# Kernel tuning notes

Measured on AMD Instinct MI355X. Metric: run time of the kernel, lower is better.

## Reference

```python
import jax, jax.numpy as jnp
import numpy as np

NUM_HEADS = 8
T = 8  # hardcoded temporal dim in the original forward
MD = 3  # max_displacement -> 7x7 window
EPS = 1e-12  # F.normalize eps


def l2_normalize(x, axis):
    n = jnp.sqrt(jnp.sum(x * x, axis=axis, keepdims=True))
    return x / jnp.maximum(n, EPS)


def correlation_7x7(q, k):
    # q, k: [B, C, H, W]; FlowNet-style correlation, kernel_size=1, max_disp=3.
    # out[b, u, v, h, w] = sum_c q[b,c,h,w] * k[b,c,h+u-3,w+v-3] (zero padded)
    B, C, H, W = q.shape
    kp = jnp.pad(k, ((0, 0), (0, 0), (MD, MD), (MD, MD)))
    outs = []
    for dy in range(2 * MD + 1):
        for dx in range(2 * MD + 1):
            ks = kp[:, :, dy:dy + H, dx:dx + W]
            outs.append(jnp.sum(q * ks, axis=1))  # [B, H, W]
    corr = jnp.stack(outs, axis=1)  # [B, 49, H, W]
    return corr.reshape(B, 2 * MD + 1, 2 * MD + 1, H, W)


def setup_inputs() -> dict:
    key = jax.random.key(0)
    ks = jax.random.split(key, 6)
    B, N, C = 8, 8192, 256
    hd = C // NUM_HEADS
    std = 0.02
    return {
        "x": jax.random.normal(ks[0], (B, N, C), dtype=jnp.float32),
        "w_qk": jax.random.normal(ks[1], (2 * C, C), dtype=jnp.float32) * std,
        "w_corr": jax.random.normal(ks[2], (hd, 49), dtype=jnp.float32) * std,
        "b_corr": jnp.zeros((hd,), dtype=jnp.float32),
        "w_proj": jax.random.normal(ks[3], (C, C), dtype=jnp.float32) * std,
        "b_proj": jnp.zeros((C,), dtype=jnp.float32),
    }


def reference(x, w_qk, w_corr, b_corr, w_proj, b_proj):
    B, N, C = x.shape
    nh = NUM_HEADS
    hd = C // nh
    H = int(np.sqrt(N // T))
    W = H

    # qk projection (no bias): [B, N, 2C] -> q, k each [B, nh, N, hd]
    qk = jnp.einsum('bnc,dc->bnd', x, w_qk)
    qk = qk.reshape(B, N, 2, nh, hd).transpose(2, 0, 3, 1, 4)
    q, k = qk[0], qk[1]

    # 'b n (t h w) d -> (b n) t d h w'
    q = q.reshape(B * nh, T, H, W, hd).transpose(0, 1, 4, 2, 3)
    k = k.reshape(B * nh, T, H, W, hd).transpose(0, 1, 4, 2, 3)

    # temporal postfix: k[t+1], last frame repeated
    k_post = jnp.concatenate([k[:, 1:], k[:, -1:]], axis=1)

    qp = q.reshape(B * nh * T, hd, H, W)
    kp = k_post.reshape(B * nh * T, hd, H, W)
    qp = l2_normalize(qp, axis=1)
    kp = l2_normalize(kp, axis=1)

    corr = correlation_7x7(qp, kp)  # [(B nh T), 7, 7, H, W]
    # 'b u v h w -> b (h w) (u v)'
    corr = corr.transpose(0, 3, 4, 1, 2).reshape(B * nh * T, H * W, 49)

    v = jnp.einsum('bpk,dk->bpd', corr, w_corr) + b_corr  # [(B nh T), HW, hd]

    # '(b n t) (h w) d -> b n (t h w) d' then 'b h n d -> b n (h d)'
    out = v.reshape(B, nh, T * H * W, hd).transpose(0, 2, 1, 3).reshape(B, N, C)
    out = jnp.einsum('bnc,dc->bnd', out, w_proj) + b_proj
    return out
```

## Files before the change

kernel.cpp:

```cpp
#include <hip/hip_runtime.h>

typedef _Float16 half8 __attribute__((ext_vector_type(8)));
typedef _Float16 half2v __attribute__((ext_vector_type(2)));
typedef float float4v __attribute__((ext_vector_type(4)));

__device__ __forceinline__ float dot2acc(unsigned a, unsigned b, float c) {
#if __has_builtin(__builtin_amdgcn_fdot2)
  return __builtin_amdgcn_fdot2(__builtin_bit_cast(half2v, a), __builtin_bit_cast(half2v, b), c, false);
#else
  half2v ha = __builtin_bit_cast(half2v, a);
  half2v hb = __builtin_bit_cast(half2v, b);
  c += (float)ha[0] * (float)hb[0];
  c += (float)ha[1] * (float)hb[1];
  return c;
#endif
}
__device__ __forceinline__ unsigned hscale(unsigned a, float s) {
  half2v ha = __builtin_bit_cast(half2v, a);
  half2v r;
  r[0] = (_Float16)((float)ha[0] * s);
  r[1] = (_Float16)((float)ha[1] * s);
  return __builtin_bit_cast(unsigned, r);
}
__device__ __forceinline__ unsigned pack2(float a, float b) {
  half2v h;
  h[0] = (_Float16)a;
  h[1] = (_Float16)b;
  return __builtin_bit_cast(unsigned, h);
}
__device__ __forceinline__ void gload_lds16(const void* g, void* l) {
  __builtin_amdgcn_global_load_lds((const __attribute__((address_space(1))) unsigned*)g,
                                   (__attribute__((address_space(3))) unsigned*)l, 16, 0, 0);
}

__global__ void cvt_all(const float4* __restrict__ x, const float4* __restrict__ wqk,
                        const float4* __restrict__ wpj,
                        ushort4* __restrict__ x16, ushort4* __restrict__ wqk16,
                        ushort4* __restrict__ wpj16) {
  int b = blockIdx.x;
  const float4* s;
  ushort4* d;
  int i;
  if (b < 16384) { s = x; d = x16; i = b * 256 + threadIdx.x; }
  else if (b < 16512) { s = wqk; d = wqk16; i = (b - 16384) * 256 + threadIdx.x; }
  else { s = wpj; d = wpj16; i = (b - 16512) * 256 + threadIdx.x; }
  float4 v = s[i];
  _Float16 a = (_Float16)v.x, bb = (_Float16)v.y, c = (_Float16)v.z, e = (_Float16)v.w;
  ushort4 o;
  o.x = __builtin_bit_cast(unsigned short, a);
  o.y = __builtin_bit_cast(unsigned short, bb);
  o.z = __builtin_bit_cast(unsigned short, c);
  o.w = __builtin_bit_cast(unsigned short, e);
  d[i] = o;
}

__global__ __launch_bounds__(256, 2)
void gemm_qk(const _Float16* __restrict__ A, const _Float16* __restrict__ Bw,
             _Float16* __restrict__ qo, _Float16* __restrict__ ko) {
  __shared__ _Float16 Ash[8192];
  __shared__ _Float16 Bsh[8192];
  const int tid = threadIdx.x;
  const int lane = tid & 63, w = tid >> 6;
  const int wm = w >> 1, wn = w & 1;
  const int ml = lane & 15, qd = lane >> 4;
  const int m0 = blockIdx.y * 128, n0 = blockIdx.x * 128;

  float4v acc[4][4];
  float4v z = {0.f, 0.f, 0.f, 0.f};
#pragma unroll
  for (int i = 0; i < 4; ++i)
#pragma unroll
    for (int j = 0; j < 4; ++j) acc[i][j] = z;

  const _Float16* Ap = A + (size_t)m0 * 256;
  const _Float16* Bp = Bw + (size_t)n0 * 256;
  const int gr = w * 64 + lane;
  const int row0 = gr >> 2, kb = gr & 3;

  {
    gload_lds16(Ap + row0 * 256 + kb * 8, Ash + (size_t)(w * 64) * 8);
    gload_lds16(Ap + (row0 + 64) * 256 + kb * 8, Ash + (size_t)(256 + w * 64) * 8);
    gload_lds16(Bp + row0 * 256 + kb * 8, Bsh + (size_t)(w * 64) * 8);
    gload_lds16(Bp + (row0 + 64) * 256 + kb * 8, Bsh + (size_t)(256 + w * 64) * 8);
  }
  __syncthreads();

#pragma unroll
  for (int kt = 0; kt < 8; ++kt) {
    const int cur = kt & 1;
    if (kt < 7) {
      const int k0 = (kt + 1) * 32;
      const int nb = (cur ^ 1) * 4096;
      gload_lds16(Ap + row0 * 256 + k0 + kb * 8, Ash + nb + (size_t)(w * 64) * 8);
      gload_lds16(Ap + (row0 + 64) * 256 + k0 + kb * 8, Ash + nb + (size_t)(256 + w * 64) * 8);
      gload_lds16(Bp + row0 * 256 + k0 + kb * 8, Bsh + nb + (size_t)(w * 64) * 8);
      gload_lds16(Bp + (row0 + 64) * 256 + k0 + kb * 8, Bsh + nb + (size_t)(256 + w * 64) * 8);
    }
    const _Float16* Ac = Ash + cur * 4096;
    const _Float16* Bc = Bsh + cur * 4096;
    half8 af[4], bf[4];
#pragma unroll
    for (int im = 0; im < 4; ++im) {
      af[im] = *(const half8*)(Ac + (wm * 64 + im * 16 + ml) * 32 + qd * 8);
      bf[im] = *(const half8*)(Bc + (wn * 64 + im * 16 + ml) * 32 + qd * 8);
    }
#pragma unroll
    for (int im = 0; im < 4; ++im)
#pragma unroll
      for (int in = 0; in < 4; ++in)
        acc[im][in] = __builtin_amdgcn_mfma_f32_16x16x32_f16(bf[in], af[im], acc[im][in], 0, 0, 0);
    __syncthreads();
  }

#pragma unroll
  for (int im = 0; im < 4; ++im) {
    int rowr = m0 + wm * 64 + im * 16 + ml;
    int b = rowr >> 13, n = rowr & 8191;
    int t = n >> 10, yx = n & 1023;
#pragma unroll
    for (int in = 0; in < 4; ++in) {
      int col = n0 + wn * 64 + in * 16 + qd * 4;
      int s = col >> 8, h = (col >> 5) & 7, j = col & 31;
      _Float16* dst = s ? ko : qo;
      int p = b * 64 + h * 8 + t;
      uint2 pk;
      pk.x = pack2(acc[im][in][0], acc[im][in][1]);
      pk.y = pack2(acc[im][in][2], acc[im][in][3]);
      *(uint2*)(dst + ((size_t)p * 1024 + yx) * 32 + j) = pk;
    }
  }
}

__global__ __launch_bounds__(256, 4)
void corr_kernel(const _Float16* __restrict__ q16, const _Float16* __restrict__ k16,
                 const float* __restrict__ wcorr, const float* __restrict__ bcorr,
                 _Float16* __restrict__ outp) {
  __shared__ uint4 smem[2304];
  __shared__ uint4 wcs[256];

  const int tid = threadIdx.x;
  const int bx = blockIdx.x;
  const int p = bx >> 2, tile = bx & 3;
  const int y0 = (tile >> 1) * 16, x0 = (tile & 1) * 16;
  const int b = p >> 6, h = (p >> 3) & 7, t = p & 7;
  const int pk = (t < 7) ? p + 1 : p;
  const int ty = tid >> 4, tx = tid & 15;

  _Float16* wch = (_Float16*)wcs;
  for (int idx = tid; idx < 2048; idx += 256) {
    int d = idx >> 6, kk = idx & 63;
    float v = (kk < 49) ? wcorr[d * 49 + kk] : (kk == 49 ? bcorr[d] : 0.f);
    wch[idx] = (_Float16)v;
  }

  const _Float16* kbase = k16 + (size_t)pk * 32768;
#pragma unroll
  for (int i = 0; i < 8; ++i) {
    int g = tid + i * 256;
    if (g < 1936) {
      int vec = g >> 2, part = g & 3;
      int ky = vec / 22, kx = vec - ky * 22;
      int gy = y0 + ky - 3, gx = x0 + kx - 3;
      uint4 val = make_uint4(0u, 0u, 0u, 0u);
      if (gy >= 0 && gy < 32 && gx >= 0 && gx < 32)
        val = *(const uint4*)(kbase + ((size_t)gy * 32 + gx) * 32 + part * 8);
      int slot = (vec << 2) | (part ^ (vec & 3) ^ ((vec >> 2) & 3));
      smem[slot] = val;
    }
  }
  __syncthreads();

  for (int v = tid; v < 484; v += 256) {
    int base = v << 2;
    int sw = (v & 3) ^ ((v >> 2) & 3);
    uint4 gg[4];
#pragma unroll
    for (int pq = 0; pq < 4; ++pq) gg[pq] = smem[base | (pq ^ sw)];
    float ss = 0.f;
#pragma unroll
    for (int pq = 0; pq < 4; ++pq) {
      const unsigned* u = (const unsigned*)&gg[pq];
#pragma unroll
      for (int e = 0; e < 4; ++e) ss = dot2acc(u[e], u[e], ss);
    }
    float sc = 1.f / fmaxf(sqrtf(ss), 1e-12f);
#pragma unroll
    for (int pq = 0; pq < 4; ++pq) {
      unsigned* u = (unsigned*)&gg[pq];
#pragma unroll
      for (int e = 0; e < 4; ++e) u[e] = hscale(u[e], sc);
      smem[base | (pq ^ sw)] = gg[pq];
    }
  }
  __syncthreads();

  const _Float16* qptr = q16 + (size_t)p * 32768 + ((size_t)(y0 + ty) * 32 + (x0 + tx)) * 32;
  uint4 qv[4];
#pragma unroll
  for (int i = 0; i < 4; ++i) qv[i] = *(const uint4*)(qptr + i * 8);
  unsigned* qu = (unsigned*)qv;
  float qss = 0.f;
#pragma unroll
  for (int e = 0; e < 16; ++e) qss = dot2acc(qu[e], qu[e], qss);
  float qsc = 1.f / fmaxf(sqrtf(qss), 1e-12f);
#pragma unroll
  for (int e = 0; e < 16; ++e) qu[e] = hscale(qu[e], qsc);

  float corr[49];
#pragma unroll
  for (int dy = 0; dy < 7; ++dy) {
#pragma unroll
    for (int dx = 0; dx < 7; ++dx) {
      int vec = (ty + dy) * 22 + (tx + dx);
      int base = vec << 2;
      int sw = (vec & 3) ^ ((vec >> 2) & 3);
      float c = 0.f;
#pragma unroll
      for (int pq = 0; pq < 4; ++pq) {
        uint4 kk = smem[base | (pq ^ sw)];
        const unsigned* ku = (const unsigned*)&kk;
#pragma unroll
        for (int e = 0; e < 4; ++e) c = dot2acc(qu[pq * 4 + e], ku[e], c);
      }
      corr[dy * 7 + dx] = c;
    }
  }
  __syncthreads();

#pragma unroll
  for (int i = 0; i < 8; ++i) {
    uint4 val;
    unsigned* vu = (unsigned*)&val;
#pragma unroll
    for (int e = 0; e < 4; ++e) {
      int idx = i * 8 + e * 2;
      half2v hh;
      hh[0] = (_Float16)(idx < 49 ? corr[idx] : (idx == 49 ? 1.f : 0.f));
      hh[1] = (_Float16)(idx + 1 < 49 ? corr[idx + 1] : (idx + 1 == 49 ? 1.f : 0.f));
      vu[e] = __builtin_bit_cast(unsigned, hh);
    }
    smem[tid * 9 + i] = val;
  }
  __syncthreads();

  _Float16* corrm = (_Float16*)smem;
  const int lane = tid & 63, w = tid >> 6;
  const int ml = lane & 15, qd = lane >> 4;
  float4v vacc[4][2];
  float4v z = {0.f, 0.f, 0.f, 0.f};
#pragma unroll
  for (int im = 0; im < 4; ++im) { vacc[im][0] = z; vacc[im][1] = z; }
#pragma unroll
  for (int ks = 0; ks < 2; ++ks) {
    half8 bfrag[2];
#pragma unroll
    for (int nt = 0; nt < 2; ++nt)
      bfrag[nt] = *(const half8*)(wch + (nt * 16 + ml) * 64 + ks * 32 + qd * 8);
#pragma unroll
    for (int im = 0; im < 4; ++im) {
      half8 afrag = *(const half8*)(corrm + (w * 64 + im * 16 + ml) * 72 + ks * 32 + qd * 8);
#pragma unroll
      for (int nt = 0; nt < 2; ++nt)
        vacc[im][nt] = __builtin_amdgcn_mfma_f32_16x16x32_f16(afrag, bfrag[nt], vacc[im][nt], 0, 0, 0);
    }
  }

#pragma unroll
  for (int im = 0; im < 4; ++im) {
#pragma unroll
    for (int nt = 0; nt < 2; ++nt) {
      int d = nt * 16 + ml;
#pragma unroll
      for (int r = 0; r < 4; ++r) {
        int pos = w * 64 + im * 16 + qd * 4 + r;
        int py = pos >> 4, px = pos & 15;
        int n = t * 1024 + (y0 + py) * 32 + (x0 + px);
        outp[(((size_t)b * 8192 + n) << 8) + h * 32 + d] = (_Float16)vacc[im][nt][r];
      }
    }
  }
}

__global__ __launch_bounds__(256, 2)
void gemm_proj(const _Float16* __restrict__ A, const _Float16* __restrict__ Bw,
               const float* __restrict__ bp, float* __restrict__ out) {
  __shared__ _Float16 Ash[8192];
  __shared__ _Float16 Bsh[8192];
  const int tid = threadIdx.x;
  const int lane = tid & 63, w = tid >> 6;
  const int wm = w >> 1, wn = w & 1;
  const int ml = lane & 15, qd = lane >> 4;
  const int m0 = blockIdx.y * 128, n0 = blockIdx.x * 128;

  float4v acc[4][4];
  float4v z = {0.f, 0.f, 0.f, 0.f};
#pragma unroll
  for (int i = 0; i < 4; ++i)
#pragma unroll
    for (int j = 0; j < 4; ++j) acc[i][j] = z;

  const _Float16* Ap = A + (size_t)m0 * 256;
  const _Float16* Bp = Bw + (size_t)n0 * 256;
  const int gr = w * 64 + lane;
  const int row0 = gr >> 2, kb = gr & 3;

  {
    gload_lds16(Ap + row0 * 256 + kb * 8, Ash + (size_t)(w * 64) * 8);
    gload_lds16(Ap + (row0 + 64) * 256 + kb * 8, Ash + (size_t)(256 + w * 64) * 8);
    gload_lds16(Bp + row0 * 256 + kb * 8, Bsh + (size_t)(w * 64) * 8);
    gload_lds16(Bp + (row0 + 64) * 256 + kb * 8, Bsh + (size_t)(256 + w * 64) * 8);
  }
  __syncthreads();

#pragma unroll
  for (int kt = 0; kt < 8; ++kt) {
    const int cur = kt & 1;
    if (kt < 7) {
      const int k0 = (kt + 1) * 32;
      const int nb = (cur ^ 1) * 4096;
      gload_lds16(Ap + row0 * 256 + k0 + kb * 8, Ash + nb + (size_t)(w * 64) * 8);
      gload_lds16(Ap + (row0 + 64) * 256 + k0 + kb * 8, Ash + nb + (size_t)(256 + w * 64) * 8);
      gload_lds16(Bp + row0 * 256 + k0 + kb * 8, Bsh + nb + (size_t)(w * 64) * 8);
      gload_lds16(Bp + (row0 + 64) * 256 + k0 + kb * 8, Bsh + nb + (size_t)(256 + w * 64) * 8);
    }
    const _Float16* Ac = Ash + cur * 4096;
    const _Float16* Bc = Bsh + cur * 4096;
    half8 af[4], bf[4];
#pragma unroll
    for (int im = 0; im < 4; ++im) {
      af[im] = *(const half8*)(Ac + (wm * 64 + im * 16 + ml) * 32 + qd * 8);
      bf[im] = *(const half8*)(Bc + (wn * 64 + im * 16 + ml) * 32 + qd * 8);
    }
#pragma unroll
    for (int im = 0; im < 4; ++im)
#pragma unroll
      for (int in = 0; in < 4; ++in)
        acc[im][in] = __builtin_amdgcn_mfma_f32_16x16x32_f16(bf[in], af[im], acc[im][in], 0, 0, 0);
    __syncthreads();
  }

#pragma unroll
  for (int im = 0; im < 4; ++im) {
    int rowr = m0 + wm * 64 + im * 16 + ml;
#pragma unroll
    for (int in = 0; in < 4; ++in) {
      int col = n0 + wn * 64 + in * 16 + qd * 4;
      float4 bb = *(const float4*)(bp + col);
      float4 o;
      o.x = acc[im][in][0] + bb.x;
      o.y = acc[im][in][1] + bb.y;
      o.z = acc[im][in][2] + bb.z;
      o.w = acc[im][in][3] + bb.w;
      *(float4*)(out + (size_t)rowr * 256 + col) = o;
    }
  }
}

extern "C" void kernel_launch(void* const* d_in, const int* in_sizes, int n_in,
                              void* d_out, int out_size, void* d_ws, size_t ws_size,
                              hipStream_t stream) {
  const float* x      = (const float*)d_in[0];
  const float* w_qk   = (const float*)d_in[1];
  const float* w_corr = (const float*)d_in[2];
  const float* b_corr = (const float*)d_in[3];
  const float* w_proj = (const float*)d_in[4];
  const float* b_proj = (const float*)d_in[5];
  float* out = (float*)d_out;

  char* ws = (char*)d_ws;
  _Float16* x16   = (_Float16*)(ws);
  _Float16* q16   = (_Float16*)(ws + 33554432);
  _Float16* k16   = (_Float16*)(ws + 67108864);
  _Float16* op16  = (_Float16*)(ws + 100663296);
  _Float16* wqk16 = (_Float16*)(ws + 134217728);
  _Float16* wpj16 = (_Float16*)(ws + 134479872);

  cvt_all<<<16576, 256, 0, stream>>>((const float4*)x, (const float4*)w_qk, (const float4*)w_proj,
                                     (ushort4*)x16, (ushort4*)wqk16, (ushort4*)wpj16);
  gemm_qk<<<dim3(4, 512), 256, 0, stream>>>(x16, wqk16, q16, k16);
  corr_kernel<<<2048, 256, 0, stream>>>(q16, k16, w_corr, b_corr, op16);
  gemm_proj<<<dim3(2, 512), 256, 0, stream>>>(op16, wpj16, b_proj, out);
}
```

Measured before the change: 230.9 us.

## Fuse x fp32-to-fp16 conversion into qk GEMM and keep full weight tile in LDS

Removes the separate conversion pass over x (64 MB read, 32 MB written, 32 MB re-read) by having gemm_qk load fp32 x rows straight from global memory and convert them to fp16 in registers. Both GEMMs now load the whole 128x256 weight slice into padded LDS once and read the A operand directly from global memory per wave, with no double-buffered A staging. Each wave owns 32 rows by 128 columns. The tradeoff is that A loads are no longer pipelined through LDS, and the larger LDS footprint (about 66 KB) may limit occupancy.

```diff
diff --git a/kernel.cpp b/kernel.cpp
--- a/kernel.cpp
+++ b/kernel.cpp
@@ -33,17 +33,14 @@
                                    (__attribute__((address_space(3))) unsigned*)l, 16, 0, 0);
 }
 
-__global__ void cvt_all(const float4* __restrict__ x, const float4* __restrict__ wqk,
-                        const float4* __restrict__ wpj,
-                        ushort4* __restrict__ x16, ushort4* __restrict__ wqk16,
-                        ushort4* __restrict__ wpj16) {
+__global__ void cvt_w(const float4* __restrict__ wqk, const float4* __restrict__ wpj,
+                      ushort4* __restrict__ wqk16, ushort4* __restrict__ wpj16) {
   int b = blockIdx.x;
   const float4* s;
   ushort4* d;
   int i;
-  if (b < 16384) { s = x; d = x16; i = b * 256 + threadIdx.x; }
-  else if (b < 16512) { s = wqk; d = wqk16; i = (b - 16384) * 256 + threadIdx.x; }
-  else { s = wpj; d = wpj16; i = (b - 16512) * 256 + threadIdx.x; }
+  if (b < 128) { s = wqk; d = wqk16; i = b * 256 + threadIdx.x; }
+  else { s = wpj; d = wpj16; i = (b - 128) * 256 + threadIdx.x; }
   float4 v = s[i];
   _Float16 a = (_Float16)v.x, bb = (_Float16)v.y, c = (_Float16)v.z, e = (_Float16)v.w;
   ushort4 o;
@@ -55,71 +52,61 @@
 }
 
 __global__ __launch_bounds__(256, 2)
-void gemm_qk(const _Float16* __restrict__ A, const _Float16* __restrict__ Bw,
+void gemm_qk(const float* __restrict__ X, const _Float16* __restrict__ Bw,
              _Float16* __restrict__ qo, _Float16* __restrict__ ko) {
-  __shared__ _Float16 Ash[8192];
-  __shared__ _Float16 Bsh[8192];
+  __shared__ _Float16 Bsh[128 * 264];
   const int tid = threadIdx.x;
   const int lane = tid & 63, w = tid >> 6;
-  const int wm = w >> 1, wn = w & 1;
   const int ml = lane & 15, qd = lane >> 4;
   const int m0 = blockIdx.y * 128, n0 = blockIdx.x * 128;
 
-  float4v acc[4][4];
+  const _Float16* Bp = Bw + (size_t)n0 * 256;
+#pragma unroll
+  for (int i = 0; i < 16; ++i) {
+    int g = tid + i * 256;
+    uint4 v = *(const uint4*)(Bp + (size_t)g * 8);
+    *(uint4*)(Bsh + (g >> 5) * 264 + (g & 31) * 8) = v;
+  }
+  __syncthreads();
+
+  float4v acc[2][8];
   float4v z = {0.f, 0.f, 0.f, 0.f};
 #pragma unroll
-  for (int i = 0; i < 4; ++i)
-#pragma unroll
-    for (int j = 0; j < 4; ++j) acc[i][j] = z;
-
-  const _Float16* Ap = A + (size_t)m0 * 256;
-  const _Float16* Bp = Bw + (size_t)n0 * 256;
-  const int gr = w * 64 + lane;
-  const int row0 = gr >> 2, kb = gr & 3;
-
-  {
-    gload_lds16(Ap + row0 * 256 + kb * 8, Ash + (size_t)(w * 64) * 8);
-    gload_lds16(Ap + (row0 + 64) * 256 + kb * 8, Ash + (size_t)(256 + w * 64) * 8);
-    gload_lds16(Bp + row0 * 256 + kb * 8, Bsh + (size_t)(w * 64) * 8);
-    gload_lds16(Bp + (row0 + 64) * 256 + kb * 8, Bsh + (size_t)(256 + w * 64) * 8);
-  }
-  __syncthreads();
-
+  for (int im = 0; im < 2; ++im)
+#pragma unroll
+    for (int in = 0; in < 8; ++in) acc[im][in] = z;
+
+  const float* Ap = X + (size_t)(m0 + w * 32) * 256;
 #pragma unroll
   for (int kt = 0; kt < 8; ++kt) {
-    const int cur = kt & 1;
-    if (kt < 7) {
-      const int k0 = (kt + 1) * 32;
-      const int nb = (cur ^ 1) * 4096;
-      gload_lds16(Ap + row0 * 256 + k0 + kb * 8, Ash + nb + (size_t)(w * 64) * 8);
-      gload_lds16(Ap + (row0 + 64) * 256 + k0 + kb * 8, Ash + nb + (size_t)(256 + w * 64) * 8);
-      gload_lds16(Bp + row0 * 256 + k0 + kb * 8, Bsh + nb + (size_t)(w * 64) * 8);
-      gload_lds16(Bp + (row0 + 64) * 256 + k0 + kb * 8, Bsh + nb + (size_t)(256 + w * 64) * 8);
-    }
-    const _Float16* Ac = Ash + cur * 4096;
-    const _Float16* Bc = Bsh + cur * 4096;
-    half8 af[4], bf[4];
-#pragma unroll
-    for (int im = 0; im < 4; ++im) {
-      af[im] = *(const half8*)(Ac + (wm * 64 + im * 16 + ml) * 32 + qd * 8);
-      bf[im] = *(const half8*)(Bc + (wn * 64 + im * 16 + ml) * 32 + qd * 8);
-    }
-#pragma unroll
-    for (int im = 0; im < 4; ++im)
-#pragma unroll
-      for (int in = 0; in < 4; ++in)
-        acc[im][in] = __builtin_amdgcn_mfma_f32_16x16x32_f16(bf[in], af[im], acc[im][in], 0, 0, 0);
-    __syncthreads();
-  }
-
-#pragma unroll
-  for (int im = 0; im < 4; ++im) {
-    int rowr = m0 + wm * 64 + im * 16 + ml;
+    half8 af[2];
+#pragma unroll
+    for (int im = 0; im < 2; ++im) {
+      const float* src = Ap + (size_t)(im * 16 + ml) * 256 + kt * 32 + qd * 8;
+      float4 f0 = *(const float4*)(src);
+      float4 f1 = *(const float4*)(src + 4);
+      half8 h;
+      h[0] = (_Float16)f0.x; h[1] = (_Float16)f0.y; h[2] = (_Float16)f0.z; h[3] = (_Float16)f0.w;
+      h[4] = (_Float16)f1.x; h[5] = (_Float16)f1.y; h[6] = (_Float16)f1.z; h[7] = (_Float16)f1.w;
+      af[im] = h;
+    }
+#pragma unroll
+    for (int in = 0; in < 8; ++in) {
+      half8 bf = *(const half8*)(Bsh + (in * 16 + ml) * 264 + kt * 32 + qd * 8);
+#pragma unroll
+      for (int im = 0; im < 2; ++im)
+        acc[im][in] = __builtin_amdgcn_mfma_f32_16x16x32_f16(bf, af[im], acc[im][in], 0, 0, 0);
+    }
+  }
+
+#pragma unroll
+  for (int im = 0; im < 2; ++im) {
+    int rowr = m0 + w * 32 + im * 16 + ml;
     int b = rowr >> 13, n = rowr & 8191;
     int t = n >> 10, yx = n & 1023;
 #pragma unroll
-    for (int in = 0; in < 4; ++in) {
-      int col = n0 + wn * 64 + in * 16 + qd * 4;
+    for (int in = 0; in < 8; ++in) {
+      int col = n0 + in * 16 + qd * 4;
       int s = col >> 8, h = (col >> 5) & 7, j = col & 31;
       _Float16* dst = s ? ko : qo;
       int p = b * 64 + h * 8 + t;
@@ -284,67 +271,50 @@
 __global__ __launch_bounds__(256, 2)
 void gemm_proj(const _Float16* __restrict__ A, const _Float16* __restrict__ Bw,
                const float* __restrict__ bp, float* __restrict__ out) {
-  __shared__ _Float16 Ash[8192];
-  __shared__ _Float16 Bsh[8192];
+  __shared__ _Float16 Bsh[128 * 264];
   const int tid = threadIdx.x;
   const int lane = tid & 63, w = tid >> 6;
-  const int wm = w >> 1, wn = w & 1;
   const int ml = lane & 15, qd = lane >> 4;
   const int m0 = blockIdx.y * 128, n0 = blockIdx.x * 128;
 
-  float4v acc[4][4];
+  const _Float16* Bp = Bw + (size_t)n0 * 256;
+#pragma unroll
+  for (int i = 0; i < 16; ++i) {
+    int g = tid + i * 256;
+    uint4 v = *(const uint4*)(Bp + (size_t)g * 8);
+    *(uint4*)(Bsh + (g >> 5) * 264 + (g & 31) * 8) = v;
+  }
+  __syncthreads();
+
+  float4v acc[2][8];
   float4v z = {0.f, 0.f, 0.f, 0.f};
 #pragma unroll
-  for (int i = 0; i < 4; ++i)
-#pragma unroll
-    for (int j = 0; j < 4; ++j) acc[i][j] = z;
-
-  const _Float16* Ap = A + (size_t)m0 * 256;
-  const _Float16* Bp = Bw + (size_t)n0 * 256;
-  const int gr = w * 64 + lane;
-  const int row0 = gr >> 2, kb = gr & 3;
-
-  {
-    gload_lds16(Ap + row0 * 256 + kb * 8, Ash + (size_t)(w * 64) * 8);
-    gload_lds16(Ap + (row0 + 64) * 256 + kb * 8, Ash + (size_t)(256 + w * 64) * 8);
-    gload_lds16(Bp + row0 * 256 + kb * 8, Bsh + (size_t)(w * 64) * 8);
-    gload_lds16(Bp + (row0 + 64) * 256 + kb * 8, Bsh + (size_t)(256 + w * 64) * 8);
-  }
-  __syncthreads();
-
+  for (int im = 0; im < 2; ++im)
+#pragma unroll
+    for (int in = 0; in < 8; ++in) acc[im][in] = z;
+
+  const _Float16* Ap = A + (size_t)(m0 + w * 32) * 256;
 #pragma unroll
   for (int kt = 0; kt < 8; ++kt) {
-    const int cur = kt & 1;
-    if (kt < 7) {
-      const int k0 = (kt + 1) * 32;
-      const int nb = (cur ^ 1) * 4096;
-      gload_lds16(Ap + row0 * 256 + k0 + kb * 8, Ash + nb + (size_t)(w * 64) * 8);
-      gload_lds16(Ap + (row0 + 64) * 256 + k0 + kb * 8, Ash + nb + (size_t)(256 + w * 64) * 8);
-      gload_lds16(Bp + row0 * 256 + k0 + kb * 8, Bsh + nb + (size_t)(w * 64) * 8);
-      gload_lds16(Bp + (row0 + 64) * 256 + k0 + kb * 8, Bsh + nb + (size_t)(256 + w * 64) * 8);
-    }
-    const _Float16* Ac = Ash + cur * 4096;
-    const _Float16* Bc = Bsh + cur * 4096;
-    half8 af[4], bf[4];
-#pragma unroll
-    for (int im = 0; im < 4; ++im) {
-      af[im] = *(const half8*)(Ac + (wm * 64 + im * 16 + ml) * 32 + qd * 8);
-      bf[im] = *(const half8*)(Bc + (wn * 64 + im * 16 + ml) * 32 + qd * 8);
-    }
-#pragma unroll
-    for (int im = 0; im < 4; ++im)
-#pragma unroll
-      for (int in = 0; in < 4; ++in)
-        acc[im][in] = __builtin_amdgcn_mfma_f32_16x16x32_f16(bf[in], af[im], acc[im][in], 0, 0, 0);
-    __syncthreads();
-  }
-
-#pragma unroll
-  for (int im = 0; im < 4; ++im) {
-    int rowr = m0 + wm * 64 + im * 16 + ml;
-#pragma unroll
-    for (int in = 0; in < 4; ++in) {
-      int col = n0 + wn * 64 + in * 16 + qd * 4;
+    half8 af[2];
+#pragma unroll
+    for (int im = 0; im < 2; ++im)
+      af[im] = *(const half8*)(Ap + (size_t)(im * 16 + ml) * 256 + kt * 32 + qd * 8);
+#pragma unroll
+    for (int in = 0; in < 8; ++in) {
+      half8 bf = *(const half8*)(Bsh + (in * 16 + ml) * 264 + kt * 32 + qd * 8);
+#pragma unroll
+      for (int im = 0; im < 2; ++im)
+        acc[im][in] = __builtin_amdgcn_mfma_f32_16x16x32_f16(bf, af[im], acc[im][in], 0, 0, 0);
+    }
+  }
+
+#pragma unroll
+  for (int im = 0; im < 2; ++im) {
+    int rowr = m0 + w * 32 + im * 16 + ml;
+#pragma unroll
+    for (int in = 0; in < 8; ++in) {
+      int col = n0 + in * 16 + qd * 4;
       float4 bb = *(const float4*)(bp + col);
       float4 o;
       o.x = acc[im][in][0] + bb.x;
@@ -368,16 +338,15 @@
   float* out = (float*)d_out;
 
   char* ws = (char*)d_ws;
-  _Float16* x16   = (_Float16*)(ws);
   _Float16* q16   = (_Float16*)(ws + 33554432);
   _Float16* k16   = (_Float16*)(ws + 67108864);
   _Float16* op16  = (_Float16*)(ws + 100663296);
   _Float16* wqk16 = (_Float16*)(ws + 134217728);
   _Float16* wpj16 = (_Float16*)(ws + 134479872);
 
-  cvt_all<<<16576, 256, 0, stream>>>((const float4*)x, (const float4*)w_qk, (const float4*)w_proj,
-                                     (ushort4*)x16, (ushort4*)wqk16, (ushort4*)wpj16);
-  gemm_qk<<<dim3(4, 512), 256, 0, stream>>>(x16, wqk16, q16, k16);
+  cvt_w<<<192, 256, 0, stream>>>((const float4*)w_qk, (const float4*)w_proj,
+                                 (ushort4*)wqk16, (ushort4*)wpj16);
+  gemm_qk<<<dim3(4, 512), 256, 0, stream>>>(x, wqk16, q16, k16);
   corr_kernel<<<2048, 256, 0, stream>>>(q16, k16, w_corr, b_corr, op16);
   gemm_proj<<<dim3(2, 512), 256, 0, stream>>>(op16, wpj16, b_proj, out);
 }
```

After: 244.0 us. +5.7%, slower.

## Widen GEMM tiles to 128x256 with 8 waves and XOR-swizzled LDS

Applied to the files above, without the earlier changes.

Both fp16 GEMMs move to 512-thread blocks that compute a 128x256 output tile, so each A tile is loaded once per block instead of once per 128-column slice. The projection GEMM now covers the full 256-wide N in one block, which halves its grid and drops redundant A reads. LDS layout gains an XOR swizzle on the 16-byte chunk index to avoid bank conflicts on the half8 fragment reads. The larger tiles mean fewer blocks in flight and a higher register and LDS footprint per block.

```diff
diff --git a/kernel.cpp b/kernel.cpp
--- a/kernel.cpp
+++ b/kernel.cpp
@@ -54,16 +54,16 @@
   d[i] = o;
 }
 
-__global__ __launch_bounds__(256, 2)
+__global__ __launch_bounds__(512, 4)
 void gemm_qk(const _Float16* __restrict__ A, const _Float16* __restrict__ Bw,
              _Float16* __restrict__ qo, _Float16* __restrict__ ko) {
-  __shared__ _Float16 Ash[8192];
-  __shared__ _Float16 Bsh[8192];
+  __shared__ _Float16 Ash[2][4096];
+  __shared__ _Float16 Bsh[2][8192];
   const int tid = threadIdx.x;
   const int lane = tid & 63, w = tid >> 6;
-  const int wm = w >> 1, wn = w & 1;
+  const int wm = w >> 2, wn = w & 3;
   const int ml = lane & 15, qd = lane >> 4;
-  const int m0 = blockIdx.y * 128, n0 = blockIdx.x * 128;
+  const int m0 = blockIdx.y * 128, n0 = blockIdx.x * 256;
 
   float4v acc[4][4];
   float4v z = {0.f, 0.f, 0.f, 0.f};
@@ -74,15 +74,12 @@
 
   const _Float16* Ap = A + (size_t)m0 * 256;
   const _Float16* Bp = Bw + (size_t)n0 * 256;
-  const int gr = w * 64 + lane;
-  const int row0 = gr >> 2, kb = gr & 3;
-
-  {
-    gload_lds16(Ap + row0 * 256 + kb * 8, Ash + (size_t)(w * 64) * 8);
-    gload_lds16(Ap + (row0 + 64) * 256 + kb * 8, Ash + (size_t)(256 + w * 64) * 8);
-    gload_lds16(Bp + row0 * 256 + kb * 8, Bsh + (size_t)(w * 64) * 8);
-    gload_lds16(Bp + (row0 + 64) * 256 + kb * 8, Bsh + (size_t)(256 + w * 64) * 8);
-  }
+  const int rA = tid >> 2, jA = (tid & 3) ^ ((rA >> 1) & 3);
+  const int rB1 = (tid + 512) >> 2, jB1 = (tid & 3) ^ ((rB1 >> 1) & 3);
+
+  gload_lds16(Ap + rA * 256 + jA * 8, &Ash[0][(size_t)(w * 64) * 8]);
+  gload_lds16(Bp + rA * 256 + jA * 8, &Bsh[0][(size_t)(w * 64) * 8]);
+  gload_lds16(Bp + rB1 * 256 + jB1 * 8, &Bsh[0][(size_t)(512 + w * 64) * 8]);
   __syncthreads();
 
 #pragma unroll
@@ -90,19 +87,18 @@
     const int cur = kt & 1;
     if (kt < 7) {
       const int k0 = (kt + 1) * 32;
-      const int nb = (cur ^ 1) * 4096;
-      gload_lds16(Ap + row0 * 256 + k0 + kb * 8, Ash + nb + (size_t)(w * 64) * 8);
-      gload_lds16(Ap + (row0 + 64) * 256 + k0 + kb * 8, Ash + nb + (size_t)(256 + w * 64) * 8);
-      gload_lds16(Bp + row0 * 256 + k0 + kb * 8, Bsh + nb + (size_t)(w * 64) * 8);
-      gload_lds16(Bp + (row0 + 64) * 256 + k0 + kb * 8, Bsh + nb + (size_t)(256 + w * 64) * 8);
-    }
-    const _Float16* Ac = Ash + cur * 4096;
-    const _Float16* Bc = Bsh + cur * 4096;
+      const int nb = cur ^ 1;
+      gload_lds16(Ap + rA * 256 + k0 + jA * 8, &Ash[nb][(size_t)(w * 64) * 8]);
+      gload_lds16(Bp + rA * 256 + k0 + jA * 8, &Bsh[nb][(size_t)(w * 64) * 8]);
+      gload_lds16(Bp + rB1 * 256 + k0 + jB1 * 8, &Bsh[nb][(size_t)(512 + w * 64) * 8]);
+    }
     half8 af[4], bf[4];
 #pragma unroll
     for (int im = 0; im < 4; ++im) {
-      af[im] = *(const half8*)(Ac + (wm * 64 + im * 16 + ml) * 32 + qd * 8);
-      bf[im] = *(const half8*)(Bc + (wn * 64 + im * 16 + ml) * 32 + qd * 8);
+      int rr = wm * 64 + im * 16 + ml;
+      af[im] = *(const half8*)(&Ash[cur][rr * 32 + (qd ^ ((rr >> 1) & 3)) * 8]);
+      int rc = wn * 64 + im * 16 + ml;
+      bf[im] = *(const half8*)(&Bsh[cur][rc * 32 + (qd ^ ((rc >> 1) & 3)) * 8]);
     }
 #pragma unroll
     for (int im = 0; im < 4; ++im)
@@ -281,16 +277,16 @@
   }
 }
 
-__global__ __launch_bounds__(256, 2)
+__global__ __launch_bounds__(512, 4)
 void gemm_proj(const _Float16* __restrict__ A, const _Float16* __restrict__ Bw,
                const float* __restrict__ bp, float* __restrict__ out) {
-  __shared__ _Float16 Ash[8192];
-  __shared__ _Float16 Bsh[8192];
+  __shared__ _Float16 Ash[2][4096];
+  __shared__ _Float16 Bsh[2][8192];
   const int tid = threadIdx.x;
   const int lane = tid & 63, w = tid >> 6;
-  const int wm = w >> 1, wn = w & 1;
+  const int wm = w >> 2, wn = w & 3;
   const int ml = lane & 15, qd = lane >> 4;
-  const int m0 = blockIdx.y * 128, n0 = blockIdx.x * 128;
+  const int m0 = blockIdx.x * 128;
 
   float4v acc[4][4];
   float4v z = {0.f, 0.f, 0.f, 0.f};
@@ -300,16 +296,13 @@
     for (int j = 0; j < 4; ++j) acc[i][j] = z;
 
   const _Float16* Ap = A + (size_t)m0 * 256;
-  const _Float16* Bp = Bw + (size_t)n0 * 256;
-  const int gr = w * 64 + lane;
-  const int row0 = gr >> 2, kb = gr & 3;
-
-  {
-    gload_lds16(Ap + row0 * 256 + kb * 8, Ash + (size_t)(w * 64) * 8);
-    gload_lds16(Ap + (row0 + 64) * 256 + kb * 8, Ash + (size_t)(256 + w * 64) * 8);
-    gload_lds16(Bp + row0 * 256 + kb * 8, Bsh + (size_t)(w * 64) * 8);
-    gload_lds16(Bp + (row0 + 64) * 256 + kb * 8, Bsh + (size_t)(256 + w * 64) * 8);
-  }
+  const _Float16* Bp = Bw;
+  const int rA = tid >> 2, jA = (tid & 3) ^ ((rA >> 1) & 3);
+  const int rB1 = (tid + 512) >> 2, jB1 = (tid & 3) ^ ((rB1 >> 1) & 3);
+
+  gload_lds16(Ap + rA * 256 + jA * 8, &Ash[0][(size_t)(w * 64) * 8]);
+  gload_lds16(Bp + rA * 256 + jA * 8, &Bsh[0][(size_t)(w * 64) * 8]);
+  gload_lds16(Bp + rB1 * 256 + jB1 * 8, &Bsh[0][(size_t)(512 + w * 64) * 8]);
   __syncthreads();
 
 #pragma unroll
@@ -317,19 +310,18 @@
     const int cur = kt & 1;
     if (kt < 7) {
       const int k0 = (kt + 1) * 32;
-      const int nb = (cur ^ 1) * 4096;
-      gload_lds16(Ap + row0 * 256 + k0 + kb * 8, Ash + nb + (size_t)(w * 64) * 8);
-      gload_lds16(Ap + (row0 + 64) * 256 + k0 + kb * 8, Ash + nb + (size_t)(256 + w * 64) * 8);
-      gload_lds16(Bp + row0 * 256 + k0 + kb * 8, Bsh + nb + (size_t)(w * 64) * 8);
-      gload_lds16(Bp + (row0 + 64) * 256 + k0 + kb * 8, Bsh + nb + (size_t)(256 + w * 64) * 8);
-    }
-    const _Float16* Ac = Ash + cur * 4096;
-    const _Float16* Bc = Bsh + cur * 4096;
+      const int nb = cur ^ 1;
+      gload_lds16(Ap + rA * 256 + k0 + jA * 8, &Ash[nb][(size_t)(w * 64) * 8]);
+      gload_lds16(Bp + rA * 256 + k0 + jA * 8, &Bsh[nb][(size_t)(w * 64) * 8]);
+      gload_lds16(Bp + rB1 * 256 + k0 + jB1 * 8, &Bsh[nb][(size_t)(512 + w * 64) * 8]);
+    }
     half8 af[4], bf[4];
 #pragma unroll
     for (int im = 0; im < 4; ++im) {
-      af[im] = *(const half8*)(Ac + (wm * 64 + im * 16 + ml) * 32 + qd * 8);
-      bf[im] = *(const half8*)(Bc + (wn * 64 + im * 16 + ml) * 32 + qd * 8);
+      int rr = wm * 64 + im * 16 + ml;
+      af[im] = *(const half8*)(&Ash[cur][rr * 32 + (qd ^ ((rr >> 1) & 3)) * 8]);
+      int rc = wn * 64 + im * 16 + ml;
+      bf[im] = *(const half8*)(&Bsh[cur][rc * 32 + (qd ^ ((rc >> 1) & 3)) * 8]);
     }
 #pragma unroll
     for (int im = 0; im < 4; ++im)
@@ -344,7 +336,7 @@
     int rowr = m0 + wm * 64 + im * 16 + ml;
 #pragma unroll
     for (int in = 0; in < 4; ++in) {
-      int col = n0 + wn * 64 + in * 16 + qd * 4;
+      int col = wn * 64 + in * 16 + qd * 4;
       float4 bb = *(const float4*)(bp + col);
       float4 o;
       o.x = acc[im][in][0] + bb.x;
@@ -377,7 +369,7 @@
 
   cvt_all<<<16576, 256, 0, stream>>>((const float4*)x, (const float4*)w_qk, (const float4*)w_proj,
                                      (ushort4*)x16, (ushort4*)wqk16, (ushort4*)wpj16);
-  gemm_qk<<<dim3(4, 512), 256, 0, stream>>>(x16, wqk16, q16, k16);
+  gemm_qk<<<dim3(2, 512), 512, 0, stream>>>(x16, wqk16, q16, k16);
   corr_kernel<<<2048, 256, 0, stream>>>(q16, k16, w_corr, b_corr, op16);
-  gemm_proj<<<dim3(2, 512), 256, 0, stream>>>(op16, wpj16, b_proj, out);
-}
+  gemm_proj<<<512, 512, 0, stream>>>(op16, wpj16, b_proj, out);
+}
```

New measurement: 225.5 us. 1.02x faster.
